# Optimization experiments

Hardware: AMD Instinct MI355X
Metric: run time of the kernel (lower is better)

Reference implementation:

```python
import jax, jax.numpy as jnp
import numpy as np

N = 8192
D = 64
HOP = 2  # -> hop_p = 3, hop_n = 3


def setup_inputs() -> dict:
    key = jax.random.key(0)
    k1, k2, k3, k4 = jax.random.split(key, 4)
    # Row-normalized positive / negative adjacency parts (dense here).
    A_p = jax.random.uniform(k1, (N, N), dtype=jnp.float32)
    A_p = A_p / jnp.sum(A_p, axis=1, keepdims=True)
    A_n = jax.random.uniform(k2, (N, N), dtype=jnp.float32)
    A_n = A_n / jnp.sum(A_n, axis=1, keepdims=True)
    x_p = jax.random.normal(k3, (N, D), dtype=jnp.float32)
    x_n = jax.random.normal(k4, (N, D), dtype=jnp.float32)
    w_p = jnp.ones((HOP + 1, 1), dtype=jnp.float32)          # _w_p, init filled with 1.0
    w_n = jnp.ones(((HOP + 1) * HOP // 2, 1), dtype=jnp.float32)  # _w_n
    return {"A_p": A_p, "A_n": A_n, "x_p": x_p, "x_n": x_n, "w_p": w_p, "w_n": w_n}


def reference(A_p, A_n, x_p, x_n, w_p, w_n):
    hop_p = HOP + 1
    feat_p = w_p[0] * x_p                # [N, D]
    feat_n = jnp.zeros_like(feat_p)
    curr_p = x_p
    curr_n_aux = x_n
    j = 0
    for h in range(hop_p):               # small fixed hop structure
        if h > 0:
            curr_p = A_p @ curr_p
            curr_n_aux = A_p @ curr_n_aux
            feat_p = feat_p + w_p[h] * curr_p
        if h != hop_p - 1:
            curr_n = A_n @ curr_n_aux
            feat_n = feat_n + w_n[j] * curr_n
            j += 1
            for _ in range(hop_p - 2 - h):
                curr_n = A_p @ curr_n
                feat_n = feat_n + w_n[j] * curr_n
                j += 1
    return jnp.concatenate([feat_p, feat_n], axis=1)  # [N, 2D]
```

## Files before the change

### kernel.cpp

```cpp
#include <hip/hip_runtime.h>
#include <hip/hip_bf16.h>
#include <stdint.h>

#define KTOT 8192
#define BM 64
#define BK 128
#define KSPLIT 4
#define KCHUNK (KTOT / KSPLIT)
#define NIT (KCHUNK / BK)

typedef __attribute__((ext_vector_type(8))) __bf16 bf16x8;
typedef __attribute__((ext_vector_type(4))) float f32x4;

__device__ __forceinline__ unsigned short f2bf(float f) {
  union { float f; unsigned int u; } a;
  a.f = f;
  unsigned int r = (a.u + 0x7fffu + ((a.u >> 16) & 1u)) >> 16;
  return (unsigned short)r;
}

__device__ __forceinline__ uint2 pack4(f32x4 v) {
  union { unsigned short h[4]; uint2 u; } pk;
  pk.h[0] = f2bf(v[0]); pk.h[1] = f2bf(v[1]);
  pk.h[2] = f2bf(v[2]); pk.h[3] = f2bf(v[3]);
  return pk.u;
}

__device__ __forceinline__ void block_bar() {
  asm volatile("s_waitcnt lgkmcnt(0)" ::: "memory");
  __builtin_amdgcn_s_barrier();
  __builtin_amdgcn_sched_barrier(0);
}

__global__ __launch_bounds__(256) void xpose_f32_bf16(const float* __restrict__ x,
                                                      __hip_bfloat16* __restrict__ xt) {
  __shared__ unsigned short tile[64][72];
  const int r0 = blockIdx.x * 64;
  const int t = threadIdx.x;
  const int a = t >> 4;
  const int c4 = (t & 15) * 4;
#pragma unroll
  for (int rep = 0; rep < 4; ++rep) {
    int r = a + rep * 16;
    f32x4 v = __builtin_nontemporal_load(
        reinterpret_cast<const f32x4*>(x + (size_t)(r0 + r) * 64 + c4));
    tile[c4 + 0][r] = f2bf(v[0]);
    tile[c4 + 1][r] = f2bf(v[1]);
    tile[c4 + 2][r] = f2bf(v[2]);
    tile[c4 + 3][r] = f2bf(v[3]);
  }
  __syncthreads();
#pragma unroll
  for (int rep = 0; rep < 4; ++rep) {
    int j = a + rep * 16;
    uint2 v = *reinterpret_cast<const uint2*>(&tile[j][c4]);
    *reinterpret_cast<uint2*>((unsigned short*)xt + (size_t)j * KTOT + r0 + c4) = v;
  }
}

__global__ __launch_bounds__(512, 4) void gemm_part(
    const float* __restrict__ A, const __hip_bfloat16* __restrict__ BTv,
    float* __restrict__ part) {
  constexpr int SZ_A = BM * BK * 2;
  __shared__ __align__(16) unsigned char smem[2 * SZ_A];
  const unsigned short* BT = (const unsigned short*)BTv;

  const int bid = blockIdx.x;
  const int kc = (bid & 7) >> 1;
  const int mblk = ((bid >> 3) << 1) | (bid & 1);
  const int r0 = mblk * BM;
  const int kbase = kc * KCHUNK;
  const int it0 = mblk & (NIT - 1);

  const int t = threadIdx.x;
  const int l = t & 63;
  const int w = t >> 6;

  const float* aptr[4];
  int loff_a[4];
#pragma unroll
  for (int r = 0; r < 4; ++r) {
    int idx = t + r * 512;
    int m = idx >> 5, c4 = idx & 31;
    aptr[r] = A + (size_t)(r0 + m) * KTOT + kbase + c4 * 4;
    loff_a[r] = m * 256 + ((c4 * 8) ^ ((m & 7) << 4));
  }

  const int lr = l & 15;
  const int g = l >> 4;
  const int col = w * 16 + lr;
  const unsigned short* bptr = BT + (size_t)col * KTOT + kbase + g * 8;
  const int asw = (lr & 7) << 4;

  f32x4 acc[4];
  const f32x4 fzero = {0.f, 0.f, 0.f, 0.f};
#pragma unroll
  for (int mt = 0; mt < 4; ++mt) acc[mt] = fzero;

  f32x4 av0[4], av1[4];
  bf16x8 Bf0[4], Bf1[4];
  unsigned char* lds0 = smem;
  unsigned char* lds1 = smem + SZ_A;

  auto kof = [&](int s) { return ((s + it0) & (NIT - 1)) * BK; };

#define LOAD_A(AV, K0)                                                        \
  _Pragma("unroll") for (int r = 0; r < 4; ++r)                               \
      AV[r] = __builtin_nontemporal_load(                                     \
          reinterpret_cast<const f32x4*>(aptr[r] + (K0)));
#define LOAD_B(BF, K0)                                                        \
  _Pragma("unroll") for (int ks = 0; ks < 4; ++ks)                            \
      BF[ks] = *reinterpret_cast<const bf16x8*>(bptr + (K0) + ks * 32);
#define WRITE_A(LDS, AV)                                                      \
  _Pragma("unroll") for (int r = 0; r < 4; ++r) {                             \
    *reinterpret_cast<uint2*>((LDS) + loff_a[r]) = pack4(AV[r]);              \
  }
#define COMPUTE(LDS, BF)                                                      \
  _Pragma("unroll") for (int ks = 0; ks < 4; ++ks) {                          \
    _Pragma("unroll") for (int mt = 0; mt < 4; ++mt) {                        \
      bf16x8 af_ = *reinterpret_cast<const bf16x8*>(                          \
          (LDS) + (mt * 16 + lr) * 256 + ((ks * 64 + g * 16) ^ asw));         \
      acc[mt] = __builtin_amdgcn_mfma_f32_16x16x32_bf16(af_, BF[ks], acc[mt], \
                                                        0, 0, 0);             \
    }                                                                         \
  }

  LOAD_A(av0, kof(0)); LOAD_B(Bf0, kof(0));
  LOAD_A(av1, kof(1)); LOAD_B(Bf1, kof(1));
  WRITE_A(lds0, av0);
  block_bar();

#pragma unroll 1
  for (int s = 0; s < NIT; s += 2) {
    if (s + 1 < NIT) { WRITE_A(lds1, av1); }
    if (s + 2 < NIT) { LOAD_A(av0, kof(s + 2)); }
    COMPUTE(lds0, Bf0);
    if (s + 2 < NIT) { LOAD_B(Bf0, kof(s + 2)); }
    if (s + 1 < NIT) block_bar();
    if (s + 1 < NIT) {
      if (s + 2 < NIT) { WRITE_A(lds0, av0); }
      if (s + 3 < NIT) { LOAD_A(av1, kof(s + 3)); }
      COMPUTE(lds1, Bf1);
      if (s + 3 < NIT) { LOAD_B(Bf1, kof(s + 3)); }
      if (s + 2 < NIT) block_bar();
    }
  }

  float* pp = part + (size_t)(kc * 128 + col) * KTOT + r0 + g * 4;
#pragma unroll
  for (int mt = 0; mt < 4; ++mt)
    __builtin_nontemporal_store(acc[mt], reinterpret_cast<f32x4*>(pp + mt * 16));
#undef LOAD_A
#undef LOAD_B
#undef WRITE_A
#undef COMPUTE
}

__global__ __launch_bounds__(256) void reduce_sep(
    const float* __restrict__ part, float* __restrict__ out,
    const float* s_lo_p, const float* s_hi_p,
    const float* __restrict__ add_ptr, const float* add_s_p,
    __hip_bfloat16* bt_lo, __hip_bfloat16* bt_hi,
    int base_lo, int base_hi, int accum) {
  const int t = threadIdx.x;
  const int col = t & 127;
  const int rbase = blockIdx.x * 32 + (t >> 7) * 16;
  const float* p0 = part + (size_t)col * KTOT + rbase;
  const bool hi = col >= 64;
  const int col64 = hi ? col - 64 : col;
  __hip_bfloat16* bt = hi ? bt_hi : bt_lo;
  const int obase = hi ? base_hi : base_lo;
  const float s = hi ? (s_hi_p ? *s_hi_p : 0.f) : (s_lo_p ? *s_lo_p : 0.f);
  const float was = add_s_p ? *add_s_p : 0.f;
#pragma unroll
  for (int i = 0; i < 4; ++i) {
    f32x4 c = __builtin_nontemporal_load(
        reinterpret_cast<const f32x4*>(p0 + 4 * i));
#pragma unroll
    for (int k = 1; k < KSPLIT; ++k)
      c += __builtin_nontemporal_load(reinterpret_cast<const f32x4*>(
          p0 + (size_t)k * 128 * KTOT + 4 * i));
    if (bt)
      *reinterpret_cast<uint2*>((unsigned short*)bt + (size_t)col64 * KTOT + rbase + 4 * i) =
          pack4(c);
    if (obase >= 0) {
#pragma unroll
      for (int j = 0; j < 4; ++j) {
        int row = rbase + 4 * i + j;
        float v = s * c[j];
        if (add_ptr && !hi) v = fmaf(was, add_ptr[(size_t)row * 64 + col64], v);
        if (accum) v += out[(size_t)row * 128 + obase + col64];
        out[(size_t)row * 128 + obase + col64] = v;
      }
    }
  }
}

__global__ __launch_bounds__(256) void reduce_comb(
    const float* __restrict__ part, float* __restrict__ out,
    const float* s_lo_p, const float* s_hi_p, __hip_bfloat16* bt_lo) {
  const int t = threadIdx.x;
  const int c = t & 63;
  const int rbase = blockIdx.x * 32 + (t >> 6) * 8;
  const float* pl = part + (size_t)c * KTOT + rbase;
  const float* ph = part + (size_t)(c + 64) * KTOT + rbase;
  const float sl = *s_lo_p, sh = *s_hi_p;
#pragma unroll
  for (int i = 0; i < 2; ++i) {
    f32x4 lo = __builtin_nontemporal_load(reinterpret_cast<const f32x4*>(pl + 4 * i));
    f32x4 hv = __builtin_nontemporal_load(reinterpret_cast<const f32x4*>(ph + 4 * i));
#pragma unroll
    for (int k = 1; k < KSPLIT; ++k) {
      lo += __builtin_nontemporal_load(reinterpret_cast<const f32x4*>(
          pl + (size_t)k * 128 * KTOT + 4 * i));
      hv += __builtin_nontemporal_load(reinterpret_cast<const f32x4*>(
          ph + (size_t)k * 128 * KTOT + 4 * i));
    }
    *reinterpret_cast<uint2*>((unsigned short*)bt_lo + (size_t)c * KTOT + rbase + 4 * i) =
        pack4(lo);
#pragma unroll
    for (int j = 0; j < 4; ++j) {
      int row = rbase + 4 * i + j;
      out[(size_t)row * 128 + 64 + c] = sl * lo[j] + sh * hv[j];
    }
  }
}

extern "C" void kernel_launch(void* const* d_in, const int* in_sizes, int n_in,
                              void* d_out, int out_size, void* d_ws, size_t ws_size,
                              hipStream_t stream) {
  const float* A_p = (const float*)d_in[0];
  const float* A_n = (const float*)d_in[1];
  const float* x_p = (const float*)d_in[2];
  const float* x_n = (const float*)d_in[3];
  const float* w_p = (const float*)d_in[4];
  const float* w_n = (const float*)d_in[5];
  float* out = (float*)d_out;

  __hip_bfloat16* BTbig = (__hip_bfloat16*)d_ws;
  __hip_bfloat16* B3T = BTbig + (size_t)192 * KTOT;
  float* part = (float*)(B3T + (size_t)128 * KTOT);

  xpose_f32_bf16<<<128, 256, 0, stream>>>(x_p, BTbig);
  xpose_f32_bf16<<<128, 256, 0, stream>>>(x_n, BTbig + (size_t)64 * KTOT);

  gemm_part<<<512, 512, 0, stream>>>(A_p, BTbig, part);
  reduce_sep<<<256, 256, 0, stream>>>(part, out, w_p + 1, nullptr, x_p, w_p + 0,
                                      B3T, BTbig + (size_t)128 * KTOT, 0, -1, 0);

  gemm_part<<<512, 512, 0, stream>>>(A_n, BTbig + (size_t)64 * KTOT, part);
  reduce_comb<<<256, 256, 0, stream>>>(part, out, w_n + 0, w_n + 2,
                                       B3T + (size_t)64 * KTOT);

  gemm_part<<<512, 512, 0, stream>>>(A_p, B3T, part);
  reduce_sep<<<256, 256, 0, stream>>>(part, out, w_p + 2, w_n + 1, nullptr, nullptr,
                                      nullptr, nullptr, 0, 64, 1);
}
```

Measured before the change: 238.5 us.

## Double K tile to 256 and restructure A/B load pipeline

Increases the K tile from 128 to 256 and rewrites the main loop. It now alternates LDS buffers with a single register stage for A, and B fragments are loaded just before compute rather than prefetched an iteration ahead. The aim is to halve barrier and loop overhead and improve A row coalescing. In exchange it doubles LDS per block, which may cut occupancy, and it exposes B load latency.

```diff
diff --git a/kernel.cpp b/kernel.cpp
--- a/kernel.cpp
+++ b/kernel.cpp
@@ -4,7 +4,7 @@
 
 #define KTOT 8192
 #define BM 64
-#define BK 128
+#define BK 256
 #define KSPLIT 4
 #define KCHUNK (KTOT / KSPLIT)
 #define NIT (KCHUNK / BK)
@@ -76,74 +76,58 @@
   const int l = t & 63;
   const int w = t >> 6;
 
-  const float* aptr[4];
-  int loff_a[4];
-#pragma unroll
-  for (int r = 0; r < 4; ++r) {
-    int idx = t + r * 512;
-    int m = idx >> 5, c4 = idx & 31;
-    aptr[r] = A + (size_t)(r0 + m) * KTOT + kbase + c4 * 4;
-    loff_a[r] = m * 256 + ((c4 * 8) ^ ((m & 7) << 4));
-  }
+  const float* abase = A + (size_t)(r0 + w) * KTOT + kbase + l * 4;
+  int loff[8];
+#pragma unroll
+  for (int r = 0; r < 8; ++r)
+    loff[r] = (w + r * 8) * 512 + ((l * 8) ^ (w << 4));
 
   const int lr = l & 15;
   const int g = l >> 4;
   const int col = w * 16 + lr;
   const unsigned short* bptr = BT + (size_t)col * KTOT + kbase + g * 8;
-  const int asw = (lr & 7) << 4;
 
   f32x4 acc[4];
   const f32x4 fzero = {0.f, 0.f, 0.f, 0.f};
 #pragma unroll
   for (int mt = 0; mt < 4; ++mt) acc[mt] = fzero;
 
-  f32x4 av0[4], av1[4];
-  bf16x8 Bf0[4], Bf1[4];
-  unsigned char* lds0 = smem;
-  unsigned char* lds1 = smem + SZ_A;
+  f32x4 av[8];
+  bf16x8 Bf[8];
 
   auto kof = [&](int s) { return ((s + it0) & (NIT - 1)) * BK; };
 
-#define LOAD_A(AV, K0)                                                        \
-  _Pragma("unroll") for (int r = 0; r < 4; ++r)                               \
-      AV[r] = __builtin_nontemporal_load(                                     \
-          reinterpret_cast<const f32x4*>(aptr[r] + (K0)));
-#define LOAD_B(BF, K0)                                                        \
-  _Pragma("unroll") for (int ks = 0; ks < 4; ++ks)                            \
-      BF[ks] = *reinterpret_cast<const bf16x8*>(bptr + (K0) + ks * 32);
-#define WRITE_A(LDS, AV)                                                      \
-  _Pragma("unroll") for (int r = 0; r < 4; ++r) {                             \
-    *reinterpret_cast<uint2*>((LDS) + loff_a[r]) = pack4(AV[r]);              \
-  }
-#define COMPUTE(LDS, BF)                                                      \
-  _Pragma("unroll") for (int ks = 0; ks < 4; ++ks) {                          \
+#define LOAD_A(K0)                                                            \
+  _Pragma("unroll") for (int r = 0; r < 8; ++r)                               \
+      av[r] = __builtin_nontemporal_load(reinterpret_cast<const f32x4*>(      \
+          abase + (size_t)r * 8 * KTOT + (K0)));
+#define LOAD_B8(K0)                                                           \
+  _Pragma("unroll") for (int ks = 0; ks < 8; ++ks)                            \
+      Bf[ks] = *reinterpret_cast<const bf16x8*>(bptr + (K0) + ks * 32);
+#define WRITE_A(LDS)                                                          \
+  _Pragma("unroll") for (int r = 0; r < 8; ++r)                               \
+      *reinterpret_cast<uint2*>((LDS) + loff[r]) = pack4(av[r]);
+#define COMPUTE(LDS)                                                          \
+  _Pragma("unroll") for (int ks = 0; ks < 8; ++ks) {                          \
     _Pragma("unroll") for (int mt = 0; mt < 4; ++mt) {                        \
       bf16x8 af_ = *reinterpret_cast<const bf16x8*>(                          \
-          (LDS) + (mt * 16 + lr) * 256 + ((ks * 64 + g * 16) ^ asw));         \
-      acc[mt] = __builtin_amdgcn_mfma_f32_16x16x32_bf16(af_, BF[ks], acc[mt], \
+          (LDS) + (mt * 16 + lr) * 512 +                                      \
+          ((ks * 64 + g * 16) ^ ((lr & 7) << 4)));                            \
+      acc[mt] = __builtin_amdgcn_mfma_f32_16x16x32_bf16(af_, Bf[ks], acc[mt], \
                                                         0, 0, 0);             \
     }                                                                         \
   }
 
-  LOAD_A(av0, kof(0)); LOAD_B(Bf0, kof(0));
-  LOAD_A(av1, kof(1)); LOAD_B(Bf1, kof(1));
-  WRITE_A(lds0, av0);
-  block_bar();
+  LOAD_A(kof(0));
 
 #pragma unroll 1
-  for (int s = 0; s < NIT; s += 2) {
-    if (s + 1 < NIT) { WRITE_A(lds1, av1); }
-    if (s + 2 < NIT) { LOAD_A(av0, kof(s + 2)); }
-    COMPUTE(lds0, Bf0);
-    if (s + 2 < NIT) { LOAD_B(Bf0, kof(s + 2)); }
-    if (s + 1 < NIT) block_bar();
-    if (s + 1 < NIT) {
-      if (s + 2 < NIT) { WRITE_A(lds0, av0); }
-      if (s + 3 < NIT) { LOAD_A(av1, kof(s + 3)); }
-      COMPUTE(lds1, Bf1);
-      if (s + 3 < NIT) { LOAD_B(Bf1, kof(s + 3)); }
-      if (s + 2 < NIT) block_bar();
-    }
+  for (int s = 0; s < NIT; ++s) {
+    unsigned char* cur = smem + (s & 1) * SZ_A;
+    WRITE_A(cur);
+    block_bar();
+    LOAD_B8(kof(s));
+    if (s + 1 < NIT) { LOAD_A(kof(s + 1)); }
+    COMPUTE(cur);
   }
 
   float* pp = part + (size_t)(kc * 128 + col) * KTOT + r0 + g * 4;
@@ -151,7 +135,7 @@
   for (int mt = 0; mt < 4; ++mt)
     __builtin_nontemporal_store(acc[mt], reinterpret_cast<f32x4*>(pp + mt * 16));
 #undef LOAD_A
-#undef LOAD_B
+#undef LOAD_B8
 #undef WRITE_A
 #undef COMPUTE
 }
```

Result: slower. 271.4 us (+13.8%).

## Halve GEMM row tile and use 4-wave blocks covering two column tiles each

Applied to the files above, without the earlier changes.

Shrinks the row tile from 64 to 32 and block size from 512 to 256 threads. Each wave now computes two 16-column groups (col and col+64) over 2 row subtiles, and the grid doubles to 1024 blocks. B fragments are no longer prefetched one stage ahead; they are loaded inside COMPUTE right before use. The aim is more, smaller blocks for better occupancy and load balance, at the cost of exposed B-load latency and twice the B traffic per unit of A.

```diff
diff --git a/kernel.cpp b/kernel.cpp
--- a/kernel.cpp
+++ b/kernel.cpp
@@ -3,7 +3,7 @@
 #include <stdint.h>
 
 #define KTOT 8192
-#define BM 64
+#define BM 32
 #define BK 128
 #define KSPLIT 4
 #define KCHUNK (KTOT / KSPLIT)
@@ -58,7 +58,7 @@
   }
 }
 
-__global__ __launch_bounds__(512, 4) void gemm_part(
+__global__ __launch_bounds__(256, 4) void gemm_part(
     const float* __restrict__ A, const __hip_bfloat16* __restrict__ BTv,
     float* __restrict__ part) {
   constexpr int SZ_A = BM * BK * 2;
@@ -77,28 +77,31 @@
   const int w = t >> 6;
 
   const float* aptr[4];
-  int loff_a[4];
+  int loff[4];
 #pragma unroll
   for (int r = 0; r < 4; ++r) {
-    int idx = t + r * 512;
+    int idx = t + r * 256;
     int m = idx >> 5, c4 = idx & 31;
     aptr[r] = A + (size_t)(r0 + m) * KTOT + kbase + c4 * 4;
-    loff_a[r] = m * 256 + ((c4 * 8) ^ ((m & 7) << 4));
+    loff[r] = m * 256 + ((c4 * 8) ^ ((m & 7) << 4));
   }
 
   const int lr = l & 15;
   const int g = l >> 4;
   const int col = w * 16 + lr;
-  const unsigned short* bptr = BT + (size_t)col * KTOT + kbase + g * 8;
+  const unsigned short* bptr0 = BT + (size_t)col * KTOT + kbase + g * 8;
+  const unsigned short* bptr1 = bptr0 + (size_t)64 * KTOT;
   const int asw = (lr & 7) << 4;
 
-  f32x4 acc[4];
+  f32x4 acc[2][2];
   const f32x4 fzero = {0.f, 0.f, 0.f, 0.f};
 #pragma unroll
-  for (int mt = 0; mt < 4; ++mt) acc[mt] = fzero;
+  for (int ct = 0; ct < 2; ++ct)
+#pragma unroll
+    for (int mt = 0; mt < 2; ++mt) acc[ct][mt] = fzero;
 
   f32x4 av0[4], av1[4];
-  bf16x8 Bf0[4], Bf1[4];
+  bf16x8 Bf[4];
   unsigned char* lds0 = smem;
   unsigned char* lds1 = smem + SZ_A;
 
@@ -108,25 +111,26 @@
   _Pragma("unroll") for (int r = 0; r < 4; ++r)                               \
       AV[r] = __builtin_nontemporal_load(                                     \
           reinterpret_cast<const f32x4*>(aptr[r] + (K0)));
-#define LOAD_B(BF, K0)                                                        \
-  _Pragma("unroll") for (int ks = 0; ks < 4; ++ks)                            \
-      BF[ks] = *reinterpret_cast<const bf16x8*>(bptr + (K0) + ks * 32);
 #define WRITE_A(LDS, AV)                                                      \
-  _Pragma("unroll") for (int r = 0; r < 4; ++r) {                             \
-    *reinterpret_cast<uint2*>((LDS) + loff_a[r]) = pack4(AV[r]);              \
-  }
-#define COMPUTE(LDS, BF)                                                      \
-  _Pragma("unroll") for (int ks = 0; ks < 4; ++ks) {                          \
-    _Pragma("unroll") for (int mt = 0; mt < 4; ++mt) {                        \
-      bf16x8 af_ = *reinterpret_cast<const bf16x8*>(                          \
-          (LDS) + (mt * 16 + lr) * 256 + ((ks * 64 + g * 16) ^ asw));         \
-      acc[mt] = __builtin_amdgcn_mfma_f32_16x16x32_bf16(af_, BF[ks], acc[mt], \
-                                                        0, 0, 0);             \
+  _Pragma("unroll") for (int r = 0; r < 4; ++r)                               \
+      *reinterpret_cast<uint2*>((LDS) + loff[r]) = pack4(AV[r]);
+#define COMPUTE(LDS, K0)                                                      \
+  _Pragma("unroll") for (int ct = 0; ct < 2; ++ct) {                          \
+    const unsigned short* bp_ = ct ? bptr1 : bptr0;                           \
+    _Pragma("unroll") for (int ks = 0; ks < 4; ++ks)                          \
+        Bf[ks] = *reinterpret_cast<const bf16x8*>(bp_ + (K0) + ks * 32);      \
+    _Pragma("unroll") for (int ks = 0; ks < 4; ++ks) {                        \
+      _Pragma("unroll") for (int mt = 0; mt < 2; ++mt) {                      \
+        bf16x8 af_ = *reinterpret_cast<const bf16x8*>(                        \
+            (LDS) + (mt * 16 + lr) * 256 + ((ks * 64 + g * 16) ^ asw));       \
+        acc[ct][mt] = __builtin_amdgcn_mfma_f32_16x16x32_bf16(                \
+            af_, Bf[ks], acc[ct][mt], 0, 0, 0);                               \
+      }                                                                       \
     }                                                                         \
   }
 
-  LOAD_A(av0, kof(0)); LOAD_B(Bf0, kof(0));
-  LOAD_A(av1, kof(1)); LOAD_B(Bf1, kof(1));
+  LOAD_A(av0, kof(0));
+  LOAD_A(av1, kof(1));
   WRITE_A(lds0, av0);
   block_bar();
 
@@ -134,24 +138,25 @@
   for (int s = 0; s < NIT; s += 2) {
     if (s + 1 < NIT) { WRITE_A(lds1, av1); }
     if (s + 2 < NIT) { LOAD_A(av0, kof(s + 2)); }
-    COMPUTE(lds0, Bf0);
-    if (s + 2 < NIT) { LOAD_B(Bf0, kof(s + 2)); }
+    COMPUTE(lds0, kof(s));
     if (s + 1 < NIT) block_bar();
     if (s + 1 < NIT) {
       if (s + 2 < NIT) { WRITE_A(lds0, av0); }
       if (s + 3 < NIT) { LOAD_A(av1, kof(s + 3)); }
-      COMPUTE(lds1, Bf1);
-      if (s + 3 < NIT) { LOAD_B(Bf1, kof(s + 3)); }
+      COMPUTE(lds1, kof(s + 1));
       if (s + 2 < NIT) block_bar();
     }
   }
 
-  float* pp = part + (size_t)(kc * 128 + col) * KTOT + r0 + g * 4;
-#pragma unroll
-  for (int mt = 0; mt < 4; ++mt)
-    __builtin_nontemporal_store(acc[mt], reinterpret_cast<f32x4*>(pp + mt * 16));
+#pragma unroll
+  for (int ct = 0; ct < 2; ++ct) {
+    float* pp = part + (size_t)(kc * 128 + col + ct * 64) * KTOT + r0 + g * 4;
+#pragma unroll
+    for (int mt = 0; mt < 2; ++mt)
+      __builtin_nontemporal_store(acc[ct][mt],
+                                  reinterpret_cast<f32x4*>(pp + mt * 16));
+  }
 #undef LOAD_A
-#undef LOAD_B
 #undef WRITE_A
 #undef COMPUTE
 }
@@ -244,15 +249,15 @@
   xpose_f32_bf16<<<128, 256, 0, stream>>>(x_p, BTbig);
   xpose_f32_bf16<<<128, 256, 0, stream>>>(x_n, BTbig + (size_t)64 * KTOT);
 
-  gemm_part<<<512, 512, 0, stream>>>(A_p, BTbig, part);
+  gemm_part<<<1024, 256, 0, stream>>>(A_p, BTbig, part);
   reduce_sep<<<256, 256, 0, stream>>>(part, out, w_p + 1, nullptr, x_p, w_p + 0,
                                       B3T, BTbig + (size_t)128 * KTOT, 0, -1, 0);
 
-  gemm_part<<<512, 512, 0, stream>>>(A_n, BTbig + (size_t)64 * KTOT, part);
+  gemm_part<<<1024, 256, 0, stream>>>(A_n, BTbig + (size_t)64 * KTOT, part);
   reduce_comb<<<256, 256, 0, stream>>>(part, out, w_n + 0, w_n + 2,
                                        B3T + (size_t)64 * KTOT);
 
-  gemm_part<<<512, 512, 0, stream>>>(A_p, B3T, part);
+  gemm_part<<<1024, 256, 0, stream>>>(A_p, B3T, part);
   reduce_sep<<<256, 256, 0, stream>>>(part, out, w_p + 2, w_n + 1, nullptr, nullptr,
                                       nullptr, nullptr, 0, 64, 1);
 }
```

Measured after the change: 335.3 us. +40.6%, slower.
